# Performance work log

Measured on AMD Instinct MI355X. Metric: run time of the kernel, lower is better.

## Reference

```python
import jax, jax.numpy as jnp
import numpy as np

B, N, C = 64, 900, 16
NCHAR, L = 75, 8
K_CLASS, K_L1, K_GIOU, K_STRING = 1.0, 5.0, 2.0, 10.0


def _pointwise_giou(p, t):
    # p, t: [..., 4] xyxy valid boxes. Elementwise GIoU == diagonal of pairwise GIoU.
    lt = jnp.maximum(p[..., :2], t[..., :2])
    rb = jnp.minimum(p[..., 2:], t[..., 2:])
    wh = jnp.clip(rb - lt, 0.0)
    inter = wh[..., 0] * wh[..., 1]
    area_p = (p[..., 2] - p[..., 0]) * (p[..., 3] - p[..., 1])
    area_t = (t[..., 2] - t[..., 0]) * (t[..., 3] - t[..., 1])
    union = area_p + area_t - inter
    iou = inter / union
    lt_c = jnp.minimum(p[..., :2], t[..., :2])
    rb_c = jnp.maximum(p[..., 2:], t[..., 2:])
    wh_c = jnp.clip(rb_c - lt_c, 0.0)
    area_c = wh_c[..., 0] * wh_c[..., 1]
    return iou - (area_c - union) / area_c


def setup_inputs() -> dict:
    key = jax.random.key(0)
    k1, k2, k3, k4, k5, k6, k7 = jax.random.split(key, 7)
    pred_logits = jax.random.normal(k1, (B, N, C), dtype=jnp.float32)
    pred_boxes = jax.random.uniform(k2, (B, N, 8), dtype=jnp.float32)
    pred_string_logits = jax.random.normal(k3, (B, NCHAR, N, L), dtype=jnp.float32)
    # valid xyxy GT boxes in [0,1]
    xy1 = jax.random.uniform(k4, (B, 2), dtype=jnp.float32) * 0.5
    wh = jax.random.uniform(k5, (B, 2), dtype=jnp.float32) * 0.5 + 1e-3
    tgt_bboxes = jnp.concatenate([xy1, xy1 + wh], axis=-1)
    plate_type = jax.random.randint(k6, (B,), 0, C, dtype=jnp.int64)
    lps = jax.random.randint(k7, (B, L), 0, NCHAR, dtype=jnp.int64)
    return {"pred_logits": pred_logits, "pred_boxes": pred_boxes,
            "pred_string_logits": pred_string_logits, "tgt_bboxes": tgt_bboxes,
            "plate_type": plate_type, "lps": lps}


def reference(pred_logits, pred_boxes, pred_string_logits, tgt_bboxes, plate_type, lps):
    # class cost: -softmax prob of target class per image
    out_prob = jax.nn.softmax(pred_logits, axis=-1)                      # [B,N,C]
    cost_class = -jnp.take_along_axis(out_prob, plate_type[:, None, None], axis=-1)[..., 0]  # [B,N]

    # vertices -> axis-aligned xyxy
    verts = pred_boxes.reshape(B, N, 4, 2)
    pred_xyxy = jnp.concatenate([verts.min(axis=2), verts.max(axis=2)], axis=-1)  # [B,N,4]

    # L1 bbox cost (cdist p=1 against the single target per image)
    cost_bbox = jnp.abs(pred_xyxy - tgt_bboxes[:, None, :]).sum(-1)      # [B,N]

    # GIoU cost (pointwise == diagonal of the original pairwise matrix)
    cost_giou = -_pointwise_giou(pred_xyxy, tgt_bboxes[:, None, :])       # [B,N]

    # string CE cost: logits [B,n_char,N,L], targets lps[B,L]
    logp = jax.nn.log_softmax(pred_string_logits, axis=1)                # [B,n_char,N,L]
    idx = jnp.broadcast_to(lps[:, None, None, :L], (B, 1, N, L))
    ce = -jnp.take_along_axis(logp, idx, axis=1)[:, 0]                   # [B,N,L]
    cost_string = ce.mean(axis=-1)                                       # [B,N]

    Cmat = (K_CLASS * cost_class + K_L1 * cost_bbox
            + K_GIOU * cost_giou + K_STRING * cost_string)               # [B,N]
    return jnp.argmin(Cmat, axis=1, keepdims=True)                       # [B,1]
```

## Files before the change

### kernel.cpp

```cpp
#include <hip/hip_runtime.h>

#define B_ 64
#define N_ 900
#define C_ 16
#define NCHAR_ 75
#define L_ 8

__global__ __launch_bounds__(256) void fused_kernel(
    const float* __restrict__ logits,
    const float* __restrict__ boxes,
    const float* __restrict__ ps,
    const float* __restrict__ tgt,
    const int*   __restrict__ ptype,
    const int*   __restrict__ lps,
    unsigned long long* __restrict__ packed,
    unsigned*           __restrict__ counter,
    int* __restrict__ out)
{
    int b     = blockIdx.x >> 2;
    int chunk = blockIdx.x & 3;
    int t     = threadIdx.x;
    int n     = chunk * 225 + t;
    bool active = (t < 225);

    unsigned long long pk = ~0ull;
    if (active) {
        int bn = b * N_ + n;

        int tl[L_];
        {
            const int4* lp4 = (const int4*)(lps + b * L_);
            int4 q0 = lp4[0], q1 = lp4[1];
            tl[0]=q0.x; tl[1]=q0.y; tl[2]=q0.z; tl[3]=q0.w;
            tl[4]=q1.x; tl[5]=q1.y; tl[6]=q1.z; tl[7]=q1.w;
        }
        float s[L_], tv[L_];
        #pragma unroll
        for (int l = 0; l < L_; ++l) { s[l] = 0.0f; tv[l] = 0.0f; }

        const float* base = ps + ((size_t)b * NCHAR_ * N_ + n) * L_;
        #pragma unroll 5
        for (int c = 0; c < NCHAR_; ++c) {
            const float4* p4 = (const float4*)(base + (size_t)c * (N_ * L_));
            float4 a = p4[0];
            float4 d = p4[1];
            s[0] += __expf(a.x); tv[0] = (c == tl[0]) ? a.x : tv[0];
            s[1] += __expf(a.y); tv[1] = (c == tl[1]) ? a.y : tv[1];
            s[2] += __expf(a.z); tv[2] = (c == tl[2]) ? a.z : tv[2];
            s[3] += __expf(a.w); tv[3] = (c == tl[3]) ? a.w : tv[3];
            s[4] += __expf(d.x); tv[4] = (c == tl[4]) ? d.x : tv[4];
            s[5] += __expf(d.y); tv[5] = (c == tl[5]) ? d.y : tv[5];
            s[6] += __expf(d.z); tv[6] = (c == tl[6]) ? d.z : tv[6];
            s[7] += __expf(d.w); tv[7] = (c == tl[7]) ? d.w : tv[7];
        }
        float ce = 0.0f;
        #pragma unroll
        for (int l = 0; l < L_; ++l) ce += __logf(s[l]) - tv[l];
        float cost_string = ce * (1.0f / L_);

        float x[C_];
        {
            const float4* lg = (const float4*)(logits + (size_t)bn * C_);
            float4 q0 = lg[0], q1 = lg[1], q2 = lg[2], q3 = lg[3];
            x[0]=q0.x; x[1]=q0.y; x[2]=q0.z; x[3]=q0.w;
            x[4]=q1.x; x[5]=q1.y; x[6]=q1.z; x[7]=q1.w;
            x[8]=q2.x; x[9]=q2.y; x[10]=q2.z; x[11]=q2.w;
            x[12]=q3.x; x[13]=q3.y; x[14]=q3.z; x[15]=q3.w;
        }
        int tcls = ptype[b];
        float m = x[0];
        #pragma unroll
        for (int i = 1; i < C_; ++i) m = fmaxf(m, x[i]);
        float se = 0.0f, xt = 0.0f;
        #pragma unroll
        for (int i = 0; i < C_; ++i) {
            se += __expf(x[i] - m);
            xt = (i == tcls) ? x[i] : xt;
        }
        float cost_class = -__expf(xt - m) / se;

        float4 tb = *(const float4*)(tgt + b * 4);
        const float4* bx = (const float4*)(boxes + (size_t)bn * 8);
        float4 w0 = bx[0], w1 = bx[1];
        float px1 = fminf(fminf(w0.x, w0.z), fminf(w1.x, w1.z));
        float py1 = fminf(fminf(w0.y, w0.w), fminf(w1.y, w1.w));
        float px2 = fmaxf(fmaxf(w0.x, w0.z), fmaxf(w1.x, w1.z));
        float py2 = fmaxf(fmaxf(w0.y, w0.w), fmaxf(w1.y, w1.w));

        float cost_bbox = fabsf(px1 - tb.x) + fabsf(py1 - tb.y)
                        + fabsf(px2 - tb.z) + fabsf(py2 - tb.w);

        float ltx = fmaxf(px1, tb.x), lty = fmaxf(py1, tb.y);
        float rbx = fminf(px2, tb.z), rby = fminf(py2, tb.w);
        float iw = fmaxf(rbx - ltx, 0.0f), ih = fmaxf(rby - lty, 0.0f);
        float inter = iw * ih;
        float area_p = (px2 - px1) * (py2 - py1);
        float area_t = (tb.z - tb.x) * (tb.w - tb.y);
        float uni = area_p + area_t - inter;
        float iou = inter / uni;
        float cx1 = fminf(px1, tb.x), cy1 = fminf(py1, tb.y);
        float cx2 = fmaxf(px2, tb.z), cy2 = fmaxf(py2, tb.w);
        float cw = fmaxf(cx2 - cx1, 0.0f), ch = fmaxf(cy2 - cy1, 0.0f);
        float area_c = cw * ch;
        float giou = iou - (area_c - uni) / area_c;

        float cost = cost_class + 5.0f * cost_bbox - 2.0f * giou + 10.0f * cost_string;

        unsigned u = __float_as_uint(cost);
        u = (u & 0x80000000u) ? ~u : (u | 0x80000000u);
        pk = ((unsigned long long)u << 32) | (unsigned)n;
    }

    __shared__ unsigned long long sp[256];
    sp[t] = pk;
    __syncthreads();
    #pragma unroll
    for (int off = 128; off > 0; off >>= 1) {
        if (t < off) {
            unsigned long long o = sp[t + off];
            if (o < sp[t]) sp[t] = o;
        }
        __syncthreads();
    }

    if (t == 0) {
        atomicMin(&packed[b], sp[0]);
        __threadfence();
        unsigned old = atomicAdd(&counter[b], 1u);
        if (old == 2u) {
            unsigned long long v = atomicAdd(&packed[b], 0ull);
            out[b] = (int)(v & 0xFFFFFFFFull);
        }
    }
}

extern "C" void kernel_launch(void* const* d_in, const int* in_sizes, int n_in,
                              void* d_out, int out_size, void* d_ws, size_t ws_size,
                              hipStream_t stream) {
    const float* logits = (const float*)d_in[0];
    const float* boxes  = (const float*)d_in[1];
    const float* ps     = (const float*)d_in[2];
    const float* tgt    = (const float*)d_in[3];
    const int*   ptype  = (const int*)d_in[4];
    const int*   lps    = (const int*)d_in[5];

    unsigned long long* packed  = (unsigned long long*)d_ws;
    unsigned*           counter = (unsigned*)((char*)d_ws + 512);
    int* out = (int*)d_out;

    hipMemsetAsync(d_ws, 0xFF, 768, stream);

    fused_kernel<<<256, 256, 0, stream>>>(
        logits, boxes, ps, tgt, ptype, lps, packed, counter, out);
}
```

Before: 35.61 us.

## Use single-wavefront blocks with shuffle argmin reduction and nontemporal loads

Replaces 256 blocks of 256 threads (with 31 idle lanes per block) with 900 one-wave blocks of 64 threads that tile B*N exactly. The shared-memory tree reduction becomes a wave-level shuffle reduction, with two separate partial minima for the blocks that straddle an image boundary. The per-image completion counter now expects a variable number of blocks. The large string-logit stream is read with nontemporal loads. This is meant to spread work across more CUs and drop the barrier overhead, at the cost of more atomics per image.

```diff
diff --git a/kernel.cpp b/kernel.cpp
--- a/kernel.cpp
+++ b/kernel.cpp
@@ -6,7 +6,9 @@
 #define NCHAR_ 75
 #define L_ 8
 
-__global__ __launch_bounds__(256) void fused_kernel(
+typedef float f32x4 __attribute__((ext_vector_type(4)));
+
+__global__ __launch_bounds__(64) void fused_kernel(
     const float* __restrict__ logits,
     const float* __restrict__ boxes,
     const float* __restrict__ ps,
@@ -17,119 +19,126 @@
     unsigned*           __restrict__ counter,
     int* __restrict__ out)
 {
-    int b     = blockIdx.x >> 2;
-    int chunk = blockIdx.x & 3;
-    int t     = threadIdx.x;
-    int n     = chunk * 225 + t;
-    bool active = (t < 225);
+    int bn = blockIdx.x * 64 + threadIdx.x;
+    int b  = bn / N_;
+    int n  = bn - b * N_;
 
-    unsigned long long pk = ~0ull;
-    if (active) {
-        int bn = b * N_ + n;
+    int tl[L_];
+    {
+        const int4* lp4 = (const int4*)(lps + b * L_);
+        int4 q0 = lp4[0], q1 = lp4[1];
+        tl[0]=q0.x; tl[1]=q0.y; tl[2]=q0.z; tl[3]=q0.w;
+        tl[4]=q1.x; tl[5]=q1.y; tl[6]=q1.z; tl[7]=q1.w;
+    }
+    float s[L_], tv[L_];
+    #pragma unroll
+    for (int l = 0; l < L_; ++l) { s[l] = 0.0f; tv[l] = 0.0f; }
 
-        int tl[L_];
-        {
-            const int4* lp4 = (const int4*)(lps + b * L_);
-            int4 q0 = lp4[0], q1 = lp4[1];
-            tl[0]=q0.x; tl[1]=q0.y; tl[2]=q0.z; tl[3]=q0.w;
-            tl[4]=q1.x; tl[5]=q1.y; tl[6]=q1.z; tl[7]=q1.w;
-        }
-        float s[L_], tv[L_];
-        #pragma unroll
-        for (int l = 0; l < L_; ++l) { s[l] = 0.0f; tv[l] = 0.0f; }
+    const float* base = ps + ((size_t)b * NCHAR_ * N_ + n) * L_;
+    #pragma unroll 5
+    for (int c = 0; c < NCHAR_; ++c) {
+        const f32x4* p4 = (const f32x4*)(base + (size_t)c * (N_ * L_));
+        f32x4 a = __builtin_nontemporal_load(p4);
+        f32x4 d = __builtin_nontemporal_load(p4 + 1);
+        s[0] += __expf(a.x); tv[0] = (c == tl[0]) ? a.x : tv[0];
+        s[1] += __expf(a.y); tv[1] = (c == tl[1]) ? a.y : tv[1];
+        s[2] += __expf(a.z); tv[2] = (c == tl[2]) ? a.z : tv[2];
+        s[3] += __expf(a.w); tv[3] = (c == tl[3]) ? a.w : tv[3];
+        s[4] += __expf(d.x); tv[4] = (c == tl[4]) ? d.x : tv[4];
+        s[5] += __expf(d.y); tv[5] = (c == tl[5]) ? d.y : tv[5];
+        s[6] += __expf(d.z); tv[6] = (c == tl[6]) ? d.z : tv[6];
+        s[7] += __expf(d.w); tv[7] = (c == tl[7]) ? d.w : tv[7];
+    }
+    float ce = 0.0f;
+    #pragma unroll
+    for (int l = 0; l < L_; ++l) ce += __logf(s[l]) - tv[l];
+    float cost_string = ce * (1.0f / L_);
 
-        const float* base = ps + ((size_t)b * NCHAR_ * N_ + n) * L_;
-        #pragma unroll 5
-        for (int c = 0; c < NCHAR_; ++c) {
-            const float4* p4 = (const float4*)(base + (size_t)c * (N_ * L_));
-            float4 a = p4[0];
-            float4 d = p4[1];
-            s[0] += __expf(a.x); tv[0] = (c == tl[0]) ? a.x : tv[0];
-            s[1] += __expf(a.y); tv[1] = (c == tl[1]) ? a.y : tv[1];
-            s[2] += __expf(a.z); tv[2] = (c == tl[2]) ? a.z : tv[2];
-            s[3] += __expf(a.w); tv[3] = (c == tl[3]) ? a.w : tv[3];
-            s[4] += __expf(d.x); tv[4] = (c == tl[4]) ? d.x : tv[4];
-            s[5] += __expf(d.y); tv[5] = (c == tl[5]) ? d.y : tv[5];
-            s[6] += __expf(d.z); tv[6] = (c == tl[6]) ? d.z : tv[6];
-            s[7] += __expf(d.w); tv[7] = (c == tl[7]) ? d.w : tv[7];
-        }
-        float ce = 0.0f;
-        #pragma unroll
-        for (int l = 0; l < L_; ++l) ce += __logf(s[l]) - tv[l];
-        float cost_string = ce * (1.0f / L_);
+    float x[C_];
+    {
+        const float4* lg = (const float4*)(logits + (size_t)bn * C_);
+        float4 q0 = lg[0], q1 = lg[1], q2 = lg[2], q3 = lg[3];
+        x[0]=q0.x; x[1]=q0.y; x[2]=q0.z; x[3]=q0.w;
+        x[4]=q1.x; x[5]=q1.y; x[6]=q1.z; x[7]=q1.w;
+        x[8]=q2.x; x[9]=q2.y; x[10]=q2.z; x[11]=q2.w;
+        x[12]=q3.x; x[13]=q3.y; x[14]=q3.z; x[15]=q3.w;
+    }
+    int tcls = ptype[b];
+    float m = x[0];
+    #pragma unroll
+    for (int i = 1; i < C_; ++i) m = fmaxf(m, x[i]);
+    float se = 0.0f, xt = 0.0f;
+    #pragma unroll
+    for (int i = 0; i < C_; ++i) {
+        se += __expf(x[i] - m);
+        xt = (i == tcls) ? x[i] : xt;
+    }
+    float cost_class = -__expf(xt - m) / se;
 
-        float x[C_];
-        {
-            const float4* lg = (const float4*)(logits + (size_t)bn * C_);
-            float4 q0 = lg[0], q1 = lg[1], q2 = lg[2], q3 = lg[3];
-            x[0]=q0.x; x[1]=q0.y; x[2]=q0.z; x[3]=q0.w;
-            x[4]=q1.x; x[5]=q1.y; x[6]=q1.z; x[7]=q1.w;
-            x[8]=q2.x; x[9]=q2.y; x[10]=q2.z; x[11]=q2.w;
-            x[12]=q3.x; x[13]=q3.y; x[14]=q3.z; x[15]=q3.w;
-        }
-        int tcls = ptype[b];
-        float m = x[0];
-        #pragma unroll
-        for (int i = 1; i < C_; ++i) m = fmaxf(m, x[i]);
-        float se = 0.0f, xt = 0.0f;
-        #pragma unroll
-        for (int i = 0; i < C_; ++i) {
-            se += __expf(x[i] - m);
-            xt = (i == tcls) ? x[i] : xt;
-        }
-        float cost_class = -__expf(xt - m) / se;
+    float4 tb = *(const float4*)(tgt + b * 4);
+    const float4* bx = (const float4*)(boxes + (size_t)bn * 8);
+    float4 w0 = bx[0], w1 = bx[1];
+    float px1 = fminf(fminf(w0.x, w0.z), fminf(w1.x, w1.z));
+    float py1 = fminf(fminf(w0.y, w0.w), fminf(w1.y, w1.w));
+    float px2 = fmaxf(fmaxf(w0.x, w0.z), fmaxf(w1.x, w1.z));
+    float py2 = fmaxf(fmaxf(w0.y, w0.w), fmaxf(w1.y, w1.w));
 
-        float4 tb = *(const float4*)(tgt + b * 4);
-        const float4* bx = (const float4*)(boxes + (size_t)bn * 8);
-        float4 w0 = bx[0], w1 = bx[1];
-        float px1 = fminf(fminf(w0.x, w0.z), fminf(w1.x, w1.z));
-        float py1 = fminf(fminf(w0.y, w0.w), fminf(w1.y, w1.w));
-        float px2 = fmaxf(fmaxf(w0.x, w0.z), fmaxf(w1.x, w1.z));
-        float py2 = fmaxf(fmaxf(w0.y, w0.w), fmaxf(w1.y, w1.w));
+    float cost_bbox = fabsf(px1 - tb.x) + fabsf(py1 - tb.y)
+                    + fabsf(px2 - tb.z) + fabsf(py2 - tb.w);
 
-        float cost_bbox = fabsf(px1 - tb.x) + fabsf(py1 - tb.y)
-                        + fabsf(px2 - tb.z) + fabsf(py2 - tb.w);
+    float ltx = fmaxf(px1, tb.x), lty = fmaxf(py1, tb.y);
+    float rbx = fminf(px2, tb.z), rby = fminf(py2, tb.w);
+    float iw = fmaxf(rbx - ltx, 0.0f), ih = fmaxf(rby - lty, 0.0f);
+    float inter = iw * ih;
+    float area_p = (px2 - px1) * (py2 - py1);
+    float area_t = (tb.z - tb.x) * (tb.w - tb.y);
+    float uni = area_p + area_t - inter;
+    float iou = inter / uni;
+    float cx1 = fminf(px1, tb.x), cy1 = fminf(py1, tb.y);
+    float cx2 = fmaxf(px2, tb.z), cy2 = fmaxf(py2, tb.w);
+    float cw = fmaxf(cx2 - cx1, 0.0f), ch = fmaxf(cy2 - cy1, 0.0f);
+    float area_c = cw * ch;
+    float giou = iou - (area_c - uni) / area_c;
 
-        float ltx = fmaxf(px1, tb.x), lty = fmaxf(py1, tb.y);
-        float rbx = fminf(px2, tb.z), rby = fminf(py2, tb.w);
-        float iw = fmaxf(rbx - ltx, 0.0f), ih = fmaxf(rby - lty, 0.0f);
-        float inter = iw * ih;
-        float area_p = (px2 - px1) * (py2 - py1);
-        float area_t = (tb.z - tb.x) * (tb.w - tb.y);
-        float uni = area_p + area_t - inter;
-        float iou = inter / uni;
-        float cx1 = fminf(px1, tb.x), cy1 = fminf(py1, tb.y);
-        float cx2 = fmaxf(px2, tb.z), cy2 = fmaxf(py2, tb.w);
-        float cw = fmaxf(cx2 - cx1, 0.0f), ch = fmaxf(cy2 - cy1, 0.0f);
-        float area_c = cw * ch;
-        float giou = iou - (area_c - uni) / area_c;
+    float cost = cost_class + 5.0f * cost_bbox - 2.0f * giou + 10.0f * cost_string;
 
-        float cost = cost_class + 5.0f * cost_bbox - 2.0f * giou + 10.0f * cost_string;
+    unsigned u = __float_as_uint(cost);
+    u = (u & 0x80000000u) ? ~u : (u | 0x80000000u);
+    unsigned long long pk = ((unsigned long long)u << 32) | (unsigned)n;
 
-        unsigned u = __float_as_uint(cost);
-        u = (u & 0x80000000u) ? ~u : (u | 0x80000000u);
-        pk = ((unsigned long long)u << 32) | (unsigned)n;
+    int b0 = (blockIdx.x * 64) / N_;
+    int b1 = (blockIdx.x * 64 + 63) / N_;
+    unsigned long long p0 = (b == b0) ? pk : ~0ull;
+    unsigned long long p1 = (b != b0) ? pk : ~0ull;
+    #pragma unroll
+    for (int off = 1; off < 64; off <<= 1) {
+        unsigned long long q0 = __shfl_xor(p0, off);
+        unsigned long long q1 = __shfl_xor(p1, off);
+        p0 = (q0 < p0) ? q0 : p0;
+        p1 = (q1 < p1) ? q1 : p1;
     }
 
-    __shared__ unsigned long long sp[256];
-    sp[t] = pk;
-    __syncthreads();
-    #pragma unroll
-    for (int off = 128; off > 0; off >>= 1) {
-        if (t < off) {
-            unsigned long long o = sp[t + off];
-            if (o < sp[t]) sp[t] = o;
+    if (threadIdx.x == 0) {
+        atomicMin(&packed[b0], p0);
+        if (b1 != b0) atomicMin(&packed[b1], p1);
+        __threadfence();
+        {
+            unsigned cnt = (unsigned)((N_ * b0 + N_ - 1) / 64 - (N_ * b0) / 64 + 1);
+            unsigned old = atomicAdd(&counter[b0], 1u);
+            if (old == cnt - 2u) {
+                __threadfence();
+                unsigned long long v = atomicAdd(&packed[b0], 0ull);
+                out[b0] = (int)(v & 0xFFFFFFFFull);
+            }
         }
-        __syncthreads();
-    }
-
-    if (t == 0) {
-        atomicMin(&packed[b], sp[0]);
-        __threadfence();
-        unsigned old = atomicAdd(&counter[b], 1u);
-        if (old == 2u) {
-            unsigned long long v = atomicAdd(&packed[b], 0ull);
-            out[b] = (int)(v & 0xFFFFFFFFull);
+        if (b1 != b0) {
+            unsigned cnt = (unsigned)((N_ * b1 + N_ - 1) / 64 - (N_ * b1) / 64 + 1);
+            unsigned old = atomicAdd(&counter[b1], 1u);
+            if (old == cnt - 2u) {
+                __threadfence();
+                unsigned long long v = atomicAdd(&packed[b1], 0ull);
+                out[b1] = (int)(v & 0xFFFFFFFFull);
+            }
         }
     }
 }
@@ -150,6 +159,6 @@
 
     hipMemsetAsync(d_ws, 0xFF, 768, stream);
 
-    fused_kernel<<<256, 256, 0, stream>>>(
+    fused_kernel<<<N_, 64, 0, stream>>>(
         logits, boxes, ps, tgt, ptype, lps, packed, counter, out);
 }
```

Measured after the change: 72.32 us. +103.1%, slower.
